# Performance work log

Hardware: AMD Instinct MI355X
Metric: run time of the kernel (lower is better)

## Reference

```python
import jax, jax.numpy as jnp
import numpy as np

NHEADS = 16
LORA_SCALE = 16.0 / 16.0  # alpha / r


def lora_linear(x, W, b, A, B):
    # base projection + low-rank LoRA path: x@W^T + b + s*(x@A^T)@B^T
    base = jnp.einsum('bse,oe->bso', x, W) + b
    low = jnp.einsum('bse,re->bsr', x, A)  # [B,S,r]
    return base + LORA_SCALE * jnp.einsum('bsr,or->bso', low, B)


def setup_inputs() -> dict:
    key = jax.random.key(0)
    E, R = 1024, 16
    ks = jax.random.split(key, 20)
    d = {'x': jax.random.normal(ks[0], (4, 1024, E), jnp.float32)}
    i = 1
    for p in ('q', 'k', 'v', 'o'):
        d[f'{p}_w'] = jax.random.normal(ks[i], (E, E), jnp.float32) * 0.02; i += 1
        d[f'{p}_b'] = jax.random.normal(ks[i], (E,), jnp.float32) * 0.02; i += 1
        d[f'{p}_la'] = jax.random.normal(ks[i], (R, E), jnp.float32) * 0.02; i += 1
        d[f'{p}_lb'] = jax.random.normal(ks[i], (E, R), jnp.float32) * 0.02; i += 1
    return d


def reference(x, q_w, q_b, q_la, q_lb, k_w, k_b, k_la, k_lb,
              v_w, v_b, v_la, v_lb, o_w, o_b, o_la, o_lb):
    B, S, E = x.shape
    H = NHEADS
    D = E // H
    q = lora_linear(x, q_w, q_b, q_la, q_lb).reshape(B, S, H, D)
    k = lora_linear(x, k_w, k_b, k_la, k_lb).reshape(B, S, H, D)
    v = lora_linear(x, v_w, v_b, v_la, v_lb).reshape(B, S, H, D)
    scores = jnp.einsum('bshd,bthd->bhst', q, k) / jnp.sqrt(jnp.asarray(D, x.dtype))
    attn = jax.nn.softmax(scores, axis=-1)
    ctx = jnp.einsum('bhst,bthd->bshd', attn, v).reshape(B, S, E)
    return lora_linear(ctx, o_w, o_b, o_la, o_lb)
```

## Files before the change

### kernel.cpp

```cpp
#include <hip/hip_runtime.h>
#include <cstdint>


typedef __attribute__((ext_vector_type(8))) short bf16x8;
typedef __attribute__((ext_vector_type(4))) float f32x4;
typedef __attribute__((ext_vector_type(16))) float f32x16;
typedef __attribute__((ext_vector_type(4))) unsigned short u16x4;
typedef __attribute__((ext_vector_type(4))) unsigned int u32x4;

__device__ __forceinline__ short f2bf(float f) {
  unsigned u = __builtin_bit_cast(unsigned, f);
  u += 0x7FFFu + ((u >> 16) & 1u);
  return (short)(u >> 16);
}

typedef __attribute__((address_space(1))) const unsigned int as1_uint;
typedef __attribute__((address_space(3))) unsigned int as3_uint;

__device__ __forceinline__ void gload_lds16(const short* g, const short* l) {
  __builtin_amdgcn_global_load_lds((as1_uint*)g,
      (as3_uint*)(unsigned int)(uintptr_t)l, 16, 0, 0);
}

__device__ __forceinline__ unsigned cvtpk(float lo, float hi) {
  unsigned r;
  asm("v_cvt_pk_bf16_f32 %0, %1, %2" : "=v"(r) : "v"(lo), "v"(hi));
  return r;
}
__device__ __forceinline__ void plswap(unsigned &a, unsigned &b) {
  asm("v_permlane32_swap_b32 %0, %1" : "+v"(a), "+v"(b));
}

__device__ __forceinline__ void build_pfrag(const f32x16 &s, bf16x8 &f0, bf16x8 &f1) {
  unsigned x0 = cvtpk(s[0], s[1]),  x1 = cvtpk(s[2], s[3]);
  unsigned x2 = cvtpk(s[4], s[5]),  x3 = cvtpk(s[6], s[7]);
  plswap(x0, x2); plswap(x1, x3);
  unsigned y0 = cvtpk(s[8], s[9]),  y1 = cvtpk(s[10], s[11]);
  unsigned y2 = cvtpk(s[12], s[13]), y3 = cvtpk(s[14], s[15]);
  plswap(y0, y2); plswap(y1, y3);
  u32x4 a = {x0, x1, x2, x3}, b = {y0, y1, y2, y3};
  f0 = __builtin_bit_cast(bf16x8, a);
  f1 = __builtin_bit_cast(bf16x8, b);
}

__global__ void prep_kernel(const float* __restrict__ x, short* __restrict__ xb,
                            const float* __restrict__ wq, const float* __restrict__ wk,
                            const float* __restrict__ wv, const float* __restrict__ wo,
                            const float* __restrict__ bq, const float* __restrict__ bk,
                            const float* __restrict__ bv, const float* __restrict__ bo,
                            const float* __restrict__ aq, const float* __restrict__ ak,
                            const float* __restrict__ av, const float* __restrict__ ao,
                            short* __restrict__ wbo) {
  const int b = blockIdx.x;
  if (b < 4096) {
    const int idx = b * 256 + threadIdx.x;
    f32x4 v = ((const f32x4*)x)[idx];
    u16x4 o;
    o[0] = (unsigned short)f2bf(v[0]);
    o[1] = (unsigned short)f2bf(v[1]);
    o[2] = (unsigned short)f2bf(v[2]);
    o[3] = (unsigned short)f2bf(v[3]);
    ((u16x4*)xb)[idx] = o;
  } else {
    const int bb = b - 4096;
    const int p = bb >> 10;
    const float* W  = (p == 0) ? wq : (p == 1) ? wk : (p == 2) ? wv : wo;
    const float* Bm = (p == 0) ? bq : (p == 1) ? bk : (p == 2) ? bv : bo;
    const float* A  = (p == 0) ? aq : (p == 1) ? ak : (p == 2) ? av : ao;
    const int idx = (bb & 1023) * 256 + threadIdx.x;
    const int n = idx >> 8;
    const int e4 = idx & 255;
    f32x4 acc = ((const f32x4*)(W + (size_t)n * 1024))[e4];
    const float* br = Bm + n * 16;
    #pragma unroll
    for (int r = 0; r < 16; ++r) {
      const f32x4 a4 = ((const f32x4*)(A + (size_t)r * 1024))[e4];
      const float bl = br[r];
      acc[0] += bl * a4[0];
      acc[1] += bl * a4[1];
      acc[2] += bl * a4[2];
      acc[3] += bl * a4[3];
    }
    u16x4 o;
    o[0] = (unsigned short)f2bf(acc[0]);
    o[1] = (unsigned short)f2bf(acc[1]);
    o[2] = (unsigned short)f2bf(acc[2]);
    o[3] = (unsigned short)f2bf(acc[3]);
    *(u16x4*)(wbo + (size_t)p * 1048576 + (size_t)idx * 4) = o;
  }
}

__device__ __forceinline__ void gemm_core_db(const short* __restrict__ xrow,
                                             const short* __restrict__ wrow,
                                             short (&As)[2][8192], short (&Bs)[2][8192],
                                             f32x4 (&acc)[4][4]) {
  const int tid = threadIdx.x;
  const int wv = tid >> 6, lane = tid & 63;
  const int wr = wv >> 1, wc = wv & 1;
  const int lrow = lane & 15, lk = lane >> 4;
  const int srow = lane >> 3, sphys = lane & 7;

#define STAGE_G(buf, kt)                                                       \
  {                                                                            \
    _Pragma("unroll")                                                          \
    for (int i = 0; i < 4; ++i) {                                              \
      const int ch = i * 4 + wv;                                               \
      const int row = ch * 8 + srow;                                           \
      const int sl = sphys ^ (row & 7);                                        \
      gload_lds16(xrow + (size_t)row * 1024 + (kt) * 64 + sl * 8, As[buf] + ch * 512); \
      gload_lds16(wrow + (size_t)row * 1024 + (kt) * 64 + sl * 8, Bs[buf] + ch * 512); \
    }                                                                          \
  }

  STAGE_G(0, 0);
  __syncthreads();
  int cur = 0;
  for (int kt = 0; kt < 16; ++kt) {
    if (kt < 15) STAGE_G(cur ^ 1, kt + 1);
    #pragma unroll
    for (int kc = 0; kc < 2; ++kc) {
      bf16x8 af[4], bw[4];
      #pragma unroll
      for (int mi = 0; mi < 4; ++mi) {
        const int row = wr * 64 + mi * 16 + lrow;
        const int slot = (kc * 4 + lk) ^ (row & 7);
        af[mi] = *(const bf16x8*)(As[cur] + row * 64 + slot * 8);
      }
      #pragma unroll
      for (int nj = 0; nj < 4; ++nj) {
        const int row = wc * 64 + nj * 16 + lrow;
        const int slot = (kc * 4 + lk) ^ (row & 7);
        bw[nj] = *(const bf16x8*)(Bs[cur] + row * 64 + slot * 8);
      }
      #pragma unroll
      for (int mi = 0; mi < 4; ++mi)
        #pragma unroll
        for (int nj = 0; nj < 4; ++nj)
          acc[mi][nj] = __builtin_amdgcn_mfma_f32_16x16x32_bf16(af[mi], bw[nj], acc[mi][nj], 0, 0, 0);
    }
    __syncthreads();
    cur ^= 1;
  }
#undef STAGE_G
}

__global__ __launch_bounds__(256)
void gemm_qkv(const short* __restrict__ xb, const short* __restrict__ wb,
              const float* __restrict__ biasq, const float* __restrict__ biask,
              const float* __restrict__ biasv,
              short* __restrict__ qbuf, short* __restrict__ kbuf, short* __restrict__ vtb) {
  __shared__ short As[2][8192];
  __shared__ short Bs[2][8192];
  const int wg = blockIdx.x;
  const int xcd = wg & 7, ix = wg >> 3;
  const int bcol = xcd * 3 + ix % 3;
  const int brow = ix / 3;
  const int p = bcol >> 3;

  const f32x4 fz = {0.f, 0.f, 0.f, 0.f};
  f32x4 acc[4][4];
  #pragma unroll
  for (int a = 0; a < 4; ++a)
    #pragma unroll
    for (int b = 0; b < 4; ++b) acc[a][b] = fz;

  gemm_core_db(xb + (size_t)brow * 128 * 1024,
               wb + (size_t)bcol * 128 * 1024, As, Bs, acc);

  const int tid = threadIdx.x;
  const int wv = tid >> 6, lane = tid & 63;
  const int wr = wv >> 1, wc = wv & 1;
  const int lrow = lane & 15, lk = lane >> 4;
  const float* bias = (p == 0) ? biasq : (p == 1) ? biask : biasv;
  const float oscale = (p == 0) ? 0.18033688f : 1.0f;
  const int c0 = (bcol & 7) * 128;
  float bcv[4];
  #pragma unroll
  for (int nj = 0; nj < 4; ++nj)
    bcv[nj] = bias[c0 + wc * 64 + nj * 16 + lrow];

  #pragma unroll
  for (int mi = 0; mi < 4; ++mi) {
    #pragma unroll
    for (int r = 0; r < 4; ++r) {
      const int gr = brow * 128 + wr * 64 + mi * 16 + lk * 4 + r;
      const int bb = gr >> 10, s = gr & 1023;
      #pragma unroll
      for (int nj = 0; nj < 4; ++nj) {
        const int gc = c0 + wc * 64 + nj * 16 + lrow;
        const float v = (acc[mi][nj][r] + bcv[nj]) * oscale;
        const int h = gc >> 6, d = gc & 63;
        const int bh = bb * 16 + h;
        if (p == 2)
          vtb[((size_t)bh * 64 + d) * 1024 + s] = f2bf(v);
        else
          ((p == 0) ? qbuf : kbuf)[((size_t)bh * 1024 + s) * 64 + d] = f2bf(v);
      }
    }
  }
}

__global__ __launch_bounds__(128)
void attn_kernel(const short* __restrict__ qbuf, const short* __restrict__ kbuf,
                 const short* __restrict__ vtb, short* __restrict__ cb) {
  __shared__ short Ks[2][64 * 64];
  __shared__ short Vs[2][64 * 64];
  const int bh = blockIdx.x, qt = blockIdx.y;
  const int tid = threadIdx.x, w = tid >> 6, lane = tid & 63;
  const int l31 = lane & 31, hi = lane >> 5;
  const int srow = lane >> 3, sphys = lane & 7;
  const short* Qp = qbuf + (size_t)bh * 65536;
  const short* Kp = kbuf + (size_t)bh * 65536;
  const short* Vp = vtb + (size_t)bh * 65536;
  const int q0 = qt * 64 + w * 32;

  bf16x8 bq[4];
  #pragma unroll
  for (int kc = 0; kc < 4; ++kc)
    bq[kc] = *(const bf16x8*)(Qp + (size_t)(q0 + l31) * 64 + kc * 16 + hi * 8);

  const f32x16 fz16 = {0.f,0.f,0.f,0.f,0.f,0.f,0.f,0.f,0.f,0.f,0.f,0.f,0.f,0.f,0.f,0.f};
  float m_run = -1e30f, l_run = 0.f;
  f32x16 acc0 = fz16, acc1 = fz16;

  #define STAGE_KV(buf, tt)                                                  \
    {                                                                        \
      const int t0s = (tt) * 64;                                             \
      _Pragma("unroll")                                                      \
      for (int i = 0; i < 4; ++i) {                                          \
        const int ch = i * 2 + w;                                            \
        const int row = ch * 8 + srow;                                       \
        const int sl = sphys ^ (row & 7);                                    \
        gload_lds16(Kp + (size_t)(t0s + row) * 64 + sl * 8, Ks[buf] + ch * 512); \
        gload_lds16(Vp + (size_t)row * 1024 + t0s + sl * 8, Vs[buf] + ch * 512); \
      }                                                                      \
    }

  STAGE_KV(0, 0);
  __syncthreads();

  int cur = 0;
  for (int tt = 0; tt < 16; ++tt) {
    if (tt < 15) STAGE_KV(cur ^ 1, tt + 1);

    f32x16 s0 = fz16, s1 = fz16;
    #pragma unroll
    for (int kc = 0; kc < 4; ++kc) {
      const int slot = (kc * 2 + hi) ^ (l31 & 7);
      const bf16x8 ak0 = *(const bf16x8*)(Ks[cur] + l31 * 64 + slot * 8);
      const bf16x8 ak1 = *(const bf16x8*)(Ks[cur] + (32 + l31) * 64 + slot * 8);
      s0 = __builtin_amdgcn_mfma_f32_32x32x16_bf16(ak0, bq[kc], s0, 0, 0, 0);
      s1 = __builtin_amdgcn_mfma_f32_32x32x16_bf16(ak1, bq[kc], s1, 0, 0, 0);
    }

    float t16[16];
    #pragma unroll
    for (int r = 0; r < 8; ++r) t16[r] = fmaxf(s0[2 * r], s0[2 * r + 1]);
    #pragma unroll
    for (int r = 0; r < 8; ++r) t16[8 + r] = fmaxf(s1[2 * r], s1[2 * r + 1]);
    #pragma unroll
    for (int r = 0; r < 8; ++r) t16[r] = fmaxf(t16[r], t16[r + 8]);
    #pragma unroll
    for (int r = 0; r < 4; ++r) t16[r] = fmaxf(t16[r], t16[r + 4]);
    float tm = fmaxf(fmaxf(t16[0], t16[1]), fmaxf(t16[2], t16[3]));
    tm = fmaxf(tm, __shfl_xor(tm, 32, 64));

    if (__any(tm - m_run > 8.0f)) {
      const float mn = fmaxf(m_run, tm);
      const float alpha = exp2f(m_run - mn);
      m_run = mn;
      l_run *= alpha;
      #pragma unroll
      for (int r = 0; r < 16; ++r) { acc0[r] *= alpha; acc1[r] *= alpha; }
    }

    float a16[16];
    #pragma unroll
    for (int r = 0; r < 16; ++r) { s0[r] = exp2f(s0[r] - m_run); }
    #pragma unroll
    for (int r = 0; r < 16; ++r) { s1[r] = exp2f(s1[r] - m_run); }
    #pragma unroll
    for (int r = 0; r < 8; ++r) a16[r] = s0[2 * r] + s0[2 * r + 1];
    #pragma unroll
    for (int r = 0; r < 8; ++r) a16[8 + r] = s1[2 * r] + s1[2 * r + 1];
    #pragma unroll
    for (int r = 0; r < 8; ++r) a16[r] += a16[r + 8];
    #pragma unroll
    for (int r = 0; r < 4; ++r) a16[r] += a16[r + 4];
    float rs = (a16[0] + a16[1]) + (a16[2] + a16[3]);
    rs += __shfl_xor(rs, 32, 64);
    l_run += rs;

    bf16x8 pf[4];
    build_pfrag(s0, pf[0], pf[1]);
    build_pfrag(s1, pf[2], pf[3]);

    #pragma unroll
    for (int kc4 = 0; kc4 < 4; ++kc4) {
      const int slot = (kc4 * 2 + hi) ^ (l31 & 7);
      const bf16x8 av0 = *(const bf16x8*)(Vs[cur] + l31 * 64 + slot * 8);
      const bf16x8 av1 = *(const bf16x8*)(Vs[cur] + (32 + l31) * 64 + slot * 8);
      acc0 = __builtin_amdgcn_mfma_f32_32x32x16_bf16(av0, pf[kc4], acc0, 0, 0, 0);
      acc1 = __builtin_amdgcn_mfma_f32_32x32x16_bf16(av1, pf[kc4], acc1, 0, 0, 0);
    }

    __syncthreads();
    cur ^= 1;
  }

  const int bb = bh >> 4, h = bh & 15;
  const int s = q0 + l31;
  short* crow = cb + (size_t)(bb * 1024 + s) * 1024 + h * 64;
  const float inv = 1.f / l_run;
  #pragma unroll
  for (int rp = 0; rp < 8; ++rp) {
    const int r = rp * 2;
    const int d = (r & 3) + 8 * (r >> 2) + 4 * hi;
    const unsigned p0 = (unsigned)(unsigned short)f2bf(acc0[r] * inv)
                      | ((unsigned)(unsigned short)f2bf(acc0[r + 1] * inv) << 16);
    const unsigned p1 = (unsigned)(unsigned short)f2bf(acc1[r] * inv)
                      | ((unsigned)(unsigned short)f2bf(acc1[r + 1] * inv) << 16);
    *(unsigned*)(crow + d) = p0;
    *(unsigned*)(crow + 32 + d) = p1;
  }
  #undef STAGE_KV
}

__device__ __forceinline__ void gemm_core_p3(const short* __restrict__ xrow,
                                             const short* __restrict__ wrow,
                                             short (&As)[3][8192], short (&Bs)[3][8192],
                                             f32x4 (&acc)[4][4]) {
  const int tid = threadIdx.x;
  const int wv = tid >> 6, lane = tid & 63;
  const int wr = wv >> 1, wc = wv & 1;
  const int lrow = lane & 15, lk = lane >> 4;
  const int srow = lane >> 3, sphys = lane & 7;

#define STAGE_G(buf, kt)                                                       \
  {                                                                            \
    _Pragma("unroll")                                                          \
    for (int i = 0; i < 4; ++i) {                                              \
      const int ch = i * 4 + wv;                                               \
      const int row = ch * 8 + srow;                                           \
      const int sl = sphys ^ (row & 7);                                        \
      gload_lds16(xrow + (size_t)row * 1024 + (kt) * 64 + sl * 8, As[buf] + ch * 512); \
      gload_lds16(wrow + (size_t)row * 1024 + (kt) * 64 + sl * 8, Bs[buf] + ch * 512); \
    }                                                                          \
  }

  STAGE_G(0, 0);
  STAGE_G(1, 1);
  int cur = 0;
  for (int kt = 0; kt < 16; ++kt) {
    if (kt < 14) {
      const int nb = (cur == 0) ? 2 : (cur - 1);
      STAGE_G(nb, kt + 2);
      asm volatile("s_waitcnt vmcnt(16)" ::: "memory");
    } else if (kt == 14) {
      asm volatile("s_waitcnt vmcnt(8)" ::: "memory");
    } else {
      asm volatile("s_waitcnt vmcnt(0)" ::: "memory");
    }
    __builtin_amdgcn_s_barrier();

    #pragma unroll
    for (int kc = 0; kc < 2; ++kc) {
      bf16x8 af[4], bw[4];
      #pragma unroll
      for (int mi = 0; mi < 4; ++mi) {
        const int row = wr * 64 + mi * 16 + lrow;
        const int slot = (kc * 4 + lk) ^ (row & 7);
        af[mi] = *(const bf16x8*)(As[cur] + row * 64 + slot * 8);
      }
      #pragma unroll
      for (int nj = 0; nj < 4; ++nj) {
        const int row = wc * 64 + nj * 16 + lrow;
        const int slot = (kc * 4 + lk) ^ (row & 7);
        bw[nj] = *(const bf16x8*)(Bs[cur] + row * 64 + slot * 8);
      }
      #pragma unroll
      for (int mi = 0; mi < 4; ++mi)
        #pragma unroll
        for (int nj = 0; nj < 4; ++nj)
          acc[mi][nj] = __builtin_amdgcn_mfma_f32_16x16x32_bf16(af[mi], bw[nj], acc[mi][nj], 0, 0, 0);
    }

    asm volatile("s_waitcnt lgkmcnt(0)" ::: "memory");
    __builtin_amdgcn_s_barrier();
    cur = (cur == 2) ? 0 : (cur + 1);
  }
#undef STAGE_G
}

__global__ __launch_bounds__(256)
void gemm_o(const short* __restrict__ cb, const short* __restrict__ wo,
            const float* __restrict__ biaso, float* __restrict__ out) {
  __shared__ short As[3][8192];
  __shared__ short Bs[3][8192];
  const int brow = blockIdx.y, bcol = blockIdx.x;
  const f32x4 fz = {0.f, 0.f, 0.f, 0.f};
  f32x4 acc[4][4];
  #pragma unroll
  for (int a = 0; a < 4; ++a)
    #pragma unroll
    for (int b = 0; b < 4; ++b) acc[a][b] = fz;

  gemm_core_p3(cb + (size_t)brow * 128 * 1024, wo + (size_t)bcol * 128 * 1024,
               As, Bs, acc);

  const int tid = threadIdx.x;
  const int wv = tid >> 6, lane = tid & 63;
  const int wr = wv >> 1, wc = wv & 1;
  const int lrow = lane & 15, lk = lane >> 4;
  float bcv[4];
  #pragma unroll
  for (int nj = 0; nj < 4; ++nj)
    bcv[nj] = biaso[bcol * 128 + wc * 64 + nj * 16 + lrow];

  #pragma unroll
  for (int mi = 0; mi < 4; ++mi) {
    #pragma unroll
    for (int r = 0; r < 4; ++r) {
      const int gr = brow * 128 + wr * 64 + mi * 16 + lk * 4 + r;
      #pragma unroll
      for (int nj = 0; nj < 4; ++nj) {
        const int gc = bcol * 128 + wc * 64 + nj * 16 + lrow;
        out[(size_t)gr * 1024 + gc] = acc[mi][nj][r] + bcv[nj];
      }
    }
  }
}

extern "C" void kernel_launch(void* const* d_in, const int* in_sizes, int n_in,
                              void* d_out, int out_size, void* d_ws, size_t ws_size,
                              hipStream_t stream) {
  (void)in_sizes; (void)n_in; (void)out_size; (void)ws_size;
  const float* x   = (const float*)d_in[0];
  const float* qw  = (const float*)d_in[1];
  const float* qb  = (const float*)d_in[2];
  const float* qla = (const float*)d_in[3];
  const float* qlb = (const float*)d_in[4];
  const float* kw  = (const float*)d_in[5];
  const float* kb  = (const float*)d_in[6];
  const float* kla = (const float*)d_in[7];
  const float* klb = (const float*)d_in[8];
  const float* vw  = (const float*)d_in[9];
  const float* vb  = (const float*)d_in[10];
  const float* vla = (const float*)d_in[11];
  const float* vlb = (const float*)d_in[12];
  const float* ow  = (const float*)d_in[13];
  const float* ob  = (const float*)d_in[14];
  const float* ola = (const float*)d_in[15];
  const float* olb = (const float*)d_in[16];

  short* xb   = (short*)d_ws;
  short* wb   = xb + (size_t)4096 * 1024;
  short* qbuf = wb + (size_t)4 * 1024 * 1024;
  short* kbuf = qbuf + (size_t)4194304;
  short* vtb  = kbuf + (size_t)4194304;

  prep_kernel<<<8192, 256, 0, stream>>>(x, xb, qw, kw, vw, ow,
                                        qlb, klb, vlb, olb,
                                        qla, kla, vla, ola, wb);
  gemm_qkv<<<768, 256, 0, stream>>>(xb, wb, qb, kb, vb, qbuf, kbuf, vtb);
  attn_kernel<<<dim3(64, 16), 128, 0, stream>>>(qbuf, kbuf, vtb, xb);
  gemm_o<<<dim3(8, 32), 256, 0, stream>>>(xb, wb + (size_t)3 * 1024 * 1024, ob, (float*)d_out);
}
```

Before: 135.0 us.

## Load K/V fragments directly from global into registers, drop LDS staging

The attention kernel no longer stages K and V tiles through shared memory with barriers. Each single-wave block (64 threads, 32 query rows) now loads K and V MFMA fragments straight from global memory into registers, ping-ponging K tiles between two register sets. The grid doubles so the number of waves stays the same. This removes LDS traffic and __syncthreads, at the cost of K/V reuse across waves: each wave reads K/V from global/L2 on its own, and more registers are live.

```diff
diff --git a/kernel.cpp b/kernel.cpp
--- a/kernel.cpp
+++ b/kernel.cpp
@@ -200,19 +200,16 @@
   }
 }
 
-__global__ __launch_bounds__(128)
+__global__ __launch_bounds__(64, 2)
 void attn_kernel(const short* __restrict__ qbuf, const short* __restrict__ kbuf,
                  const short* __restrict__ vtb, short* __restrict__ cb) {
-  __shared__ short Ks[2][64 * 64];
-  __shared__ short Vs[2][64 * 64];
   const int bh = blockIdx.x, qt = blockIdx.y;
-  const int tid = threadIdx.x, w = tid >> 6, lane = tid & 63;
+  const int lane = threadIdx.x;
   const int l31 = lane & 31, hi = lane >> 5;
-  const int srow = lane >> 3, sphys = lane & 7;
   const short* Qp = qbuf + (size_t)bh * 65536;
   const short* Kp = kbuf + (size_t)bh * 65536;
   const short* Vp = vtb + (size_t)bh * 65536;
-  const int q0 = qt * 64 + w * 32;
+  const int q0 = qt * 32;
 
   bf16x8 bq[4];
   #pragma unroll
@@ -223,90 +220,69 @@
   float m_run = -1e30f, l_run = 0.f;
   f32x16 acc0 = fz16, acc1 = fz16;
 
-  #define STAGE_KV(buf, tt)                                                  \
-    {                                                                        \
-      const int t0s = (tt) * 64;                                             \
-      _Pragma("unroll")                                                      \
-      for (int i = 0; i < 4; ++i) {                                          \
-        const int ch = i * 2 + w;                                            \
-        const int row = ch * 8 + srow;                                       \
-        const int sl = sphys ^ (row & 7);                                    \
-        gload_lds16(Kp + (size_t)(t0s + row) * 64 + sl * 8, Ks[buf] + ch * 512); \
-        gload_lds16(Vp + (size_t)row * 1024 + t0s + sl * 8, Vs[buf] + ch * 512); \
-      }                                                                      \
-    }
-
-  STAGE_KV(0, 0);
-  __syncthreads();
-
-  int cur = 0;
-  for (int tt = 0; tt < 16; ++tt) {
-    if (tt < 15) STAGE_KV(cur ^ 1, tt + 1);
-
-    f32x16 s0 = fz16, s1 = fz16;
-    #pragma unroll
-    for (int kc = 0; kc < 4; ++kc) {
-      const int slot = (kc * 2 + hi) ^ (l31 & 7);
-      const bf16x8 ak0 = *(const bf16x8*)(Ks[cur] + l31 * 64 + slot * 8);
-      const bf16x8 ak1 = *(const bf16x8*)(Ks[cur] + (32 + l31) * 64 + slot * 8);
-      s0 = __builtin_amdgcn_mfma_f32_32x32x16_bf16(ak0, bq[kc], s0, 0, 0, 0);
-      s1 = __builtin_amdgcn_mfma_f32_32x32x16_bf16(ak1, bq[kc], s1, 0, 0, 0);
-    }
-
-    float t16[16];
-    #pragma unroll
-    for (int r = 0; r < 8; ++r) t16[r] = fmaxf(s0[2 * r], s0[2 * r + 1]);
-    #pragma unroll
-    for (int r = 0; r < 8; ++r) t16[8 + r] = fmaxf(s1[2 * r], s1[2 * r + 1]);
-    #pragma unroll
-    for (int r = 0; r < 8; ++r) t16[r] = fmaxf(t16[r], t16[r + 8]);
-    #pragma unroll
-    for (int r = 0; r < 4; ++r) t16[r] = fmaxf(t16[r], t16[r + 4]);
-    float tm = fmaxf(fmaxf(t16[0], t16[1]), fmaxf(t16[2], t16[3]));
-    tm = fmaxf(tm, __shfl_xor(tm, 32, 64));
-
-    if (__any(tm - m_run > 8.0f)) {
-      const float mn = fmaxf(m_run, tm);
-      const float alpha = exp2f(m_run - mn);
-      m_run = mn;
-      l_run *= alpha;
-      #pragma unroll
-      for (int r = 0; r < 16; ++r) { acc0[r] *= alpha; acc1[r] *= alpha; }
-    }
-
-    float a16[16];
-    #pragma unroll
-    for (int r = 0; r < 16; ++r) { s0[r] = exp2f(s0[r] - m_run); }
-    #pragma unroll
-    for (int r = 0; r < 16; ++r) { s1[r] = exp2f(s1[r] - m_run); }
-    #pragma unroll
-    for (int r = 0; r < 8; ++r) a16[r] = s0[2 * r] + s0[2 * r + 1];
-    #pragma unroll
-    for (int r = 0; r < 8; ++r) a16[8 + r] = s1[2 * r] + s1[2 * r + 1];
-    #pragma unroll
-    for (int r = 0; r < 8; ++r) a16[r] += a16[r + 8];
-    #pragma unroll
-    for (int r = 0; r < 4; ++r) a16[r] += a16[r + 4];
-    float rs = (a16[0] + a16[1]) + (a16[2] + a16[3]);
-    rs += __shfl_xor(rs, 32, 64);
-    l_run += rs;
-
-    bf16x8 pf[4];
-    build_pfrag(s0, pf[0], pf[1]);
-    build_pfrag(s1, pf[2], pf[3]);
-
-    #pragma unroll
-    for (int kc4 = 0; kc4 < 4; ++kc4) {
-      const int slot = (kc4 * 2 + hi) ^ (l31 & 7);
-      const bf16x8 av0 = *(const bf16x8*)(Vs[cur] + l31 * 64 + slot * 8);
-      const bf16x8 av1 = *(const bf16x8*)(Vs[cur] + (32 + l31) * 64 + slot * 8);
-      acc0 = __builtin_amdgcn_mfma_f32_32x32x16_bf16(av0, pf[kc4], acc0, 0, 0, 0);
-      acc1 = __builtin_amdgcn_mfma_f32_32x32x16_bf16(av1, pf[kc4], acc1, 0, 0, 0);
-    }
-
-    __syncthreads();
-    cur ^= 1;
-  }
+#define LOADK(tt, KA)                                                          \
+  { _Pragma("unroll")                                                          \
+    for (int kc = 0; kc < 4; ++kc) {                                           \
+      KA[kc][0] = *(const bf16x8*)(Kp + (size_t)((tt) * 64 + l31) * 64 + kc * 16 + hi * 8);      \
+      KA[kc][1] = *(const bf16x8*)(Kp + (size_t)((tt) * 64 + 32 + l31) * 64 + kc * 16 + hi * 8); \
+    } }
+
+#define TILE_BODY(tt, KA)                                                      \
+  { bf16x8 va[4][2];                                                           \
+    _Pragma("unroll")                                                          \
+    for (int kc = 0; kc < 4; ++kc) {                                           \
+      va[kc][0] = *(const bf16x8*)(Vp + (size_t)l31 * 1024 + (tt) * 64 + kc * 16 + hi * 8);        \
+      va[kc][1] = *(const bf16x8*)(Vp + (size_t)(32 + l31) * 1024 + (tt) * 64 + kc * 16 + hi * 8); \
+    }                                                                          \
+    f32x16 s0 = fz16, s1 = fz16;                                               \
+    _Pragma("unroll")                                                          \
+    for (int kc = 0; kc < 4; ++kc) {                                           \
+      s0 = __builtin_amdgcn_mfma_f32_32x32x16_bf16(KA[kc][0], bq[kc], s0, 0, 0, 0); \
+      s1 = __builtin_amdgcn_mfma_f32_32x32x16_bf16(KA[kc][1], bq[kc], s1, 0, 0, 0); \
+    }                                                                          \
+    float t16[16];                                                             \
+    _Pragma("unroll") for (int r = 0; r < 8; ++r) t16[r] = fmaxf(s0[2*r], s0[2*r+1]);     \
+    _Pragma("unroll") for (int r = 0; r < 8; ++r) t16[8+r] = fmaxf(s1[2*r], s1[2*r+1]);   \
+    _Pragma("unroll") for (int r = 0; r < 8; ++r) t16[r] = fmaxf(t16[r], t16[r+8]);       \
+    _Pragma("unroll") for (int r = 0; r < 4; ++r) t16[r] = fmaxf(t16[r], t16[r+4]);       \
+    float tm = fmaxf(fmaxf(t16[0], t16[1]), fmaxf(t16[2], t16[3]));            \
+    tm = fmaxf(tm, __shfl_xor(tm, 32, 64));                                    \
+    if (__any(tm - m_run > 8.0f)) {                                            \
+      const float mn = fmaxf(m_run, tm);                                       \
+      const float alpha = exp2f(m_run - mn);                                   \
+      m_run = mn; l_run *= alpha;                                              \
+      _Pragma("unroll") for (int r = 0; r < 16; ++r) { acc0[r] *= alpha; acc1[r] *= alpha; } \
+    }                                                                          \
+    float a16[16];                                                             \
+    _Pragma("unroll") for (int r = 0; r < 16; ++r) s0[r] = exp2f(s0[r] - m_run); \
+    _Pragma("unroll") for (int r = 0; r < 16; ++r) s1[r] = exp2f(s1[r] - m_run); \
+    _Pragma("unroll") for (int r = 0; r < 8; ++r) a16[r] = s0[2*r] + s0[2*r+1];   \
+    _Pragma("unroll") for (int r = 0; r < 8; ++r) a16[8+r] = s1[2*r] + s1[2*r+1]; \
+    _Pragma("unroll") for (int r = 0; r < 8; ++r) a16[r] += a16[r+8];          \
+    _Pragma("unroll") for (int r = 0; r < 4; ++r) a16[r] += a16[r+4];          \
+    float rs = (a16[0] + a16[1]) + (a16[2] + a16[3]);                          \
+    rs += __shfl_xor(rs, 32, 64);                                              \
+    l_run += rs;                                                               \
+    bf16x8 pf[4];                                                              \
+    build_pfrag(s0, pf[0], pf[1]);                                             \
+    build_pfrag(s1, pf[2], pf[3]);                                             \
+    _Pragma("unroll")                                                          \
+    for (int kc = 0; kc < 4; ++kc) {                                           \
+      acc0 = __builtin_amdgcn_mfma_f32_32x32x16_bf16(va[kc][0], pf[kc], acc0, 0, 0, 0); \
+      acc1 = __builtin_amdgcn_mfma_f32_32x32x16_bf16(va[kc][1], pf[kc], acc1, 0, 0, 0); \
+    } }
+
+  bf16x8 kA[4][2], kB[4][2];
+  LOADK(0, kA)
+  for (int t2 = 0; t2 < 8; ++t2) {
+    const int tt = t2 * 2;
+    LOADK(tt + 1, kB)
+    TILE_BODY(tt, kA)
+    if (t2 < 7) LOADK(tt + 2, kA)
+    TILE_BODY(tt + 1, kB)
+  }
+#undef LOADK
+#undef TILE_BODY
 
   const int bb = bh >> 4, h = bh & 15;
   const int s = q0 + l31;
@@ -323,7 +299,6 @@
     *(unsigned*)(crow + d) = p0;
     *(unsigned*)(crow + 32 + d) = p1;
   }
-  #undef STAGE_KV
 }
 
 __device__ __forceinline__ void gemm_core_p3(const short* __restrict__ xrow,
@@ -463,6 +438,6 @@
                                         qlb, klb, vlb, olb,
                                         qla, kla, vla, ola, wb);
   gemm_qkv<<<768, 256, 0, stream>>>(xb, wb, qb, kb, vb, qbuf, kbuf, vtb);
-  attn_kernel<<<dim3(64, 16), 128, 0, stream>>>(qbuf, kbuf, vtb, xb);
+  attn_kernel<<<dim3(64, 32), 64, 0, stream>>>(qbuf, kbuf, vtb, xb);
   gemm_o<<<dim3(8, 32), 256, 0, stream>>>(xb, wb + (size_t)3 * 1024 * 1024, ob, (float*)d_out);
 }
```

Result: slower. 156.0 us (+15.5%).
